# Kernel optimization log

Hardware: AMD Instinct MI355X
Metric: run time of the kernel (lower is better)

Reference implementation:

```python
import jax, jax.numpy as jnp
import numpy as np

N_NODES = 50000
N_EDGES = 800000
D = 128
L = 3


def setup_inputs() -> dict:
    key = jax.random.key(0)
    ks = jax.random.split(key, 8)
    h = jax.random.normal(ks[0], (N_NODES, D), dtype=jnp.float32)
    src = jax.random.randint(ks[1], (N_EDGES,), 0, N_NODES, dtype=jnp.int32)
    dst = jax.random.randint(ks[2], (N_EDGES,), 0, N_NODES, dtype=jnp.int32)
    # MLP weights per GIN layer, scaled ~Glorot to keep activations bounded across layers
    w_scale = 0.05
    W1 = jax.random.normal(ks[3], (L, D, D), dtype=jnp.float32) * w_scale
    b1 = jnp.zeros((L, D), dtype=jnp.float32)
    W2 = jax.random.normal(ks[4], (L, D, D), dtype=jnp.float32) * w_scale
    b2 = jnp.zeros((L, D), dtype=jnp.float32)
    eps = jnp.zeros((L,), dtype=jnp.float32)  # init_eps=0, learnable
    return {"h": h, "src": src, "dst": dst, "W1": W1, "b1": b1, "W2": W2, "b2": b2, "eps": eps}


def reference(h, src, dst, W1, b1, W2, b2, eps):
    # GIN: h <- MLP((1 + eps) * h + sum_{(u->v) in E} h_u) per layer (sum aggregation)
    n = h.shape[0]
    for l in range(W1.shape[0]):
        agg = jax.ops.segment_sum(h[src], dst, num_segments=n)  # [N, D]
        z = (1.0 + eps[l]) * h + agg
        hid = jnp.maximum(z @ W1[l] + b1[l], 0.0)  # Linear + ReLU
        h = hid @ W2[l] + b2[l]                    # Linear
    return h
```

## Files before the change

kernel.cpp:

```cpp
#include <hip/hip_runtime.h>
#include <hip/hip_bf16.h>
#include <stdint.h>

#define N_NODES 50000
#define N_EDGES 800000
#define D 128
#define NLAYER 3
#define NGROUP (N_NODES / 16)
#define CAPG 384
#define GSTRIDE 384
#define MAXCH 12

#define NBKT2 196
#define BCAP 4608
#define EPB_A 2048
#define PA_BLOCKS ((N_EDGES + EPB_A - 1) / EPB_A)

typedef __attribute__((ext_vector_type(8))) short bf16x8;
typedef __attribute__((ext_vector_type(4))) float f32x4;

__device__ __forceinline__ short f2bf(float f) {
    union { float f; uint32_t u; } v; v.f = f;
    uint32_t u = v.u;
    uint32_t r = u + 0x7fffu + ((u >> 16) & 1u);
    return (short)(r >> 16);
}
__device__ __forceinline__ float bf2f(short s) {
    union { uint32_t u; float f; } v;
    v.u = ((uint32_t)(uint16_t)s) << 16;
    return v.f;
}

__global__ void wconv(const float* __restrict__ W1, const float* __restrict__ W2,
                      short* __restrict__ Wswz) {
    int t = blockIdx.x * blockDim.x + threadIdx.x;
    if (t >= NLAYER * 2 * 4 * 8 * 64) return;
    int lane = t & 63;
    int nt   = (t >> 6) & 7;
    int ks   = (t >> 9) & 3;
    int mat  = (t >> 11) & 1;
    int l    = t >> 12;
    const float* W = (mat == 0 ? W1 : W2) + (size_t)l * D * D;
    int n = nt * 16 + (lane & 15);
    short* outp = Wswz + (size_t)t * 8;
#pragma unroll
    for (int j = 0; j < 8; ++j) {
        int k = ks * 32 + (lane >> 4) * 8 + j;
        outp[j] = f2bf(W[k * D + n]);
    }
}

__global__ void h2bf(const float* __restrict__ h, short* __restrict__ hbf) {
    int t = blockIdx.x * blockDim.x + threadIdx.x;
    if (t >= N_NODES * D / 8) return;
    f32x4 a = ((const f32x4*)h)[2 * t];
    f32x4 b = ((const f32x4*)h)[2 * t + 1];
    bf16x8 o;
    o[0] = f2bf(a.x); o[1] = f2bf(a.y); o[2] = f2bf(a.z); o[3] = f2bf(a.w);
    o[4] = f2bf(b.x); o[5] = f2bf(b.y); o[6] = f2bf(b.z); o[7] = f2bf(b.w);
    ((bf16x8*)hbf)[t] = o;
}

__global__ void zero_bcur(int* __restrict__ bcur) {
    if (threadIdx.x < NBKT2) bcur[threadIdx.x] = 0;
}

__global__ __launch_bounds__(256) void packA(const int* __restrict__ src,
                                             const int* __restrict__ dst,
                                             int* __restrict__ bcur,
                                             int* __restrict__ epack) {
    __shared__ int hcnt[NBKT2];
    __shared__ int hbase[NBKT2];
    if (threadIdx.x < NBKT2) hcnt[threadIdx.x] = 0;
    __syncthreads();
    int base = blockIdx.x * EPB_A;
    int end = base + EPB_A; if (end > N_EDGES) end = N_EDGES;
    for (int e = base + threadIdx.x; e < end; e += 256)
        atomicAdd(&hcnt[dst[e] >> 8], 1);
    __syncthreads();
    if (threadIdx.x < NBKT2) {
        int c = hcnt[threadIdx.x];
        hbase[threadIdx.x] = c ? atomicAdd(&bcur[threadIdx.x], c) : 0;
        hcnt[threadIdx.x] = 0;
    }
    __syncthreads();
    for (int e = base + threadIdx.x; e < end; e += 256) {
        int s = src[e], d = dst[e];
        int b = d >> 8;
        int r = atomicAdd(&hcnt[b], 1);
        int slot = hbase[b] + r;
        if (slot < BCAP)
            epack[(size_t)b * BCAP + slot] = (s << 8) | (d & 255);
    }
}

__global__ __launch_bounds__(256) void segB(const int* __restrict__ epack,
                                            const int* __restrict__ bcur,
                                            int* __restrict__ esd,
                                            int* __restrict__ gcnt) {
    __shared__ int image[16 * GSTRIDE];
    __shared__ int cur[16];
    const int b = blockIdx.x;
    int n = bcur[b]; if (n > BCAP) n = BCAP;
    const int* ep = epack + (size_t)b * BCAP;
    const int nG = (NGROUP - b * 16 < 16) ? (NGROUP - b * 16) : 16;

    for (int i = threadIdx.x; i < 16 * GSTRIDE; i += 256) image[i] = 0x80;
    if (threadIdx.x < 16) cur[threadIdx.x] = 0;
    __syncthreads();
    for (int i = threadIdx.x; i < n; i += 256) {
        int e = ep[i];
        int g = (e >> 4) & 15;
        int r = atomicAdd(&cur[g], 1);
        if (r < CAPG) image[g * GSTRIDE + r] = e & ~0xF0;
    }
    __syncthreads();
    if (threadIdx.x < nG) {
        int c = cur[threadIdx.x];
        gcnt[b * 16 + threadIdx.x] = (c > CAPG) ? CAPG : c;
    }
    for (int i = threadIdx.x; i < nG * GSTRIDE; i += 256)
        esd[(size_t)(b * 16) * GSTRIDE + i] = image[i];
}

__global__ __launch_bounds__(256) void gin_layer(const short* __restrict__ hbf,
                                                 const int* __restrict__ gcnt,
                                                 const int* __restrict__ esd,
                                                 const short* __restrict__ Wl,
                                                 const float* __restrict__ b1,
                                                 const float* __restrict__ b2,
                                                 const float* __restrict__ eps, int l,
                                                 float* __restrict__ outf,
                                                 short* __restrict__ outbf, int last) {
    __shared__ union {
        short stg[3][4096];
        struct { short zl[2048]; short hl[2048]; } t;
    } sm;
    __shared__ __align__(8) unsigned char dmask[512];

    const int lane = threadIdx.x & 63;
    const int wid  = threadIdx.x >> 6;
    const int g    = blockIdx.x;
    const int n0   = g * 16;
    const int m    = lane & 15;
    const int kh   = lane >> 4;

    const char* hby = (const char*)hbf;
    const int lo  = g * GSTRIDE;
    int cnt = gcnt[g]; if (cnt > CAPG) cnt = CAPG;
    const int nch = (cnt + 31) >> 5;
    const uint32_t one = 0x3F80u;

    const int sl = lane >> 2;
    const int wq = wid * 64 + (lane & 3) * 16;

    const uint32_t stg_base =
        (uint32_t)(uintptr_t)(__attribute__((address_space(3))) short*)&sm.stg[0][0];

    f32x4 acc[2];
    acc[0] = (f32x4)(0.0f); acc[1] = (f32x4)(0.0f);

#define STAGE(b, rA, rB) do { \
        __builtin_amdgcn_global_load_lds( \
            (const __attribute__((address_space(1))) void*)(hby + (uint32_t)((rA) & ~0xFF) + wq), \
            (__attribute__((address_space(3))) void*)(&sm.stg[(b)][0] + wid * 1024), 16, 0, 0); \
        __builtin_amdgcn_global_load_lds( \
            (const __attribute__((address_space(1))) void*)(hby + (uint32_t)((rB) & ~0xFF) + wq), \
            (__attribute__((address_space(3))) void*)(&sm.stg[(b)][0] + wid * 1024 + 512), 16, 0, 0); \
    } while (0)

    const int* ep = esd + lo;

    int esvA[MAXCH], esvB[MAXCH];
#pragma unroll
    for (int c = 0; c < MAXCH; ++c) {
        esvA[c] = ep[c * 32 + sl];
        esvB[c] = ep[c * 32 + 16 + sl];
    }

    STAGE(0, esvA[0], esvB[0]);
    STAGE(1, esvA[1], esvB[1]);

    if (wid == 0 && (lane & 3) == 0) {
        const int sA = sl, sB = 16 + sl;
        const int pA = ((sA >> 1) & 3) * 8 + 2 * (sA >> 3) + (sA & 1);
        const int pB = ((sB >> 1) & 3) * 8 + 2 * (sB >> 3) + (sB & 1);
#pragma unroll
        for (int c = 0; c < MAXCH; ++c) {
            dmask[c * 32 + pA] = (unsigned char)(esvA[c] & 0xFF);
            dmask[c * 32 + pB] = (unsigned char)(esvB[c] & 0xFF);
        }
    }
    asm volatile("s_waitcnt lgkmcnt(0)" ::: "memory");
    __builtin_amdgcn_s_barrier();

#pragma unroll
    for (int c = 0; c < MAXCH; ++c) {
        if (c >= nch) break;
        if (c + 2 < nch) {
            STAGE((c + 2) % 3, esvA[c + 2], esvB[c + 2]);
            asm volatile("s_waitcnt vmcnt(4)" ::: "memory");
        } else if (c + 1 < nch) {
            asm volatile("s_waitcnt vmcnt(2)" ::: "memory");
        } else {
            asm volatile("s_waitcnt vmcnt(0)" ::: "memory");
        }
        __builtin_amdgcn_sched_barrier(0);

        uint32_t breg = stg_base + (uint32_t)((c % 3) * 8192 + wid * 2048) + lane * 8;
        uint64_t t0, t1, t2, t3;
        asm volatile("ds_read_b64_tr_b16 %0, %1"             : "=v"(t0) : "v"(breg));
        asm volatile("ds_read_b64_tr_b16 %0, %1 offset:512"  : "=v"(t1) : "v"(breg));
        asm volatile("ds_read_b64_tr_b16 %0, %1 offset:1024" : "=v"(t2) : "v"(breg));
        asm volatile("ds_read_b64_tr_b16 %0, %1 offset:1536" : "=v"(t3) : "v"(breg));
        uint2 dm = *(const uint2*)&dmask[c * 32 + kh * 8];
        asm volatile("s_waitcnt lgkmcnt(0)" ::: "memory");
        __builtin_amdgcn_sched_barrier(0);

        union U64 { uint64_t u; uint32_t d[2]; };
        U64 p0, p1, p2, p3; p0.u = t0; p1.u = t1; p2.u = t2; p3.u = t3;
        union { uint32_t w[4]; bf16x8 v; } bf0, bf1;
        bf0.w[0] = (p0.d[0] & 0xFFFFu) | (p0.d[1] << 16);
        bf1.w[0] = (p0.d[0] >> 16) | (p0.d[1] & 0xFFFF0000u);
        bf0.w[1] = (p1.d[0] & 0xFFFFu) | (p1.d[1] << 16);
        bf1.w[1] = (p1.d[0] >> 16) | (p1.d[1] & 0xFFFF0000u);
        bf0.w[2] = (p2.d[0] & 0xFFFFu) | (p2.d[1] << 16);
        bf1.w[2] = (p2.d[0] >> 16) | (p2.d[1] & 0xFFFF0000u);
        bf0.w[3] = (p3.d[0] & 0xFFFFu) | (p3.d[1] << 16);
        bf1.w[3] = (p3.d[0] >> 16) | (p3.d[1] & 0xFFFF0000u);

        bf16x8 am;
#pragma unroll
        for (int e = 0; e < 4; ++e) {
            am[e]     = (((dm.x >> (e * 8)) & 255u) == (uint32_t)m) ? (short)one : (short)0;
            am[e + 4] = (((dm.y >> (e * 8)) & 255u) == (uint32_t)m) ? (short)one : (short)0;
        }
        acc[0] = __builtin_amdgcn_mfma_f32_16x16x32_bf16(am, bf0.v, acc[0], 0, 0, 0);
        acc[1] = __builtin_amdgcn_mfma_f32_16x16x32_bf16(am, bf1.v, acc[1], 0, 0, 0);
    }

    {
        const float se = 1.0f + eps[l];
#pragma unroll
        for (int t = 0; t < 2; ++t) {
            int col = (wid * 2 + t) * 16 + m;
#pragma unroll
            for (int r = 0; r < 4; ++r) {
                int row = n0 + kh * 4 + r;
                acc[t][r] += se * bf2f(hbf[(size_t)row * D + col]);
            }
        }
    }

    __syncthreads();

#pragma unroll
    for (int t = 0; t < 2; ++t) {
        int col = (wid * 2 + t) * 16 + m;
        int gi = col >> 3, ci = col & 7;
#pragma unroll
        for (int r = 0; r < 4; ++r) {
            int row = kh * 4 + r;
            sm.t.zl[row * 128 + ((gi ^ (row & 7)) << 3) + ci] = f2bf(acc[t][r]);
        }
    }
    __syncthreads();

    f32x4 acc1[2];
    acc1[0] = (f32x4)(0.0f); acc1[1] = (f32x4)(0.0f);
#pragma unroll
    for (int ks = 0; ks < 4; ++ks) {
        int gidx = ks * 4 + kh;
        bf16x8 af = *(const bf16x8*)&sm.t.zl[m * 128 + ((gidx ^ (m & 7)) * 8)];
#pragma unroll
        for (int t = 0; t < 2; ++t) {
            int nt = wid * 2 + t;
            bf16x8 bf = *(const bf16x8*)(Wl + ((size_t)(ks * 8 + nt) * 64 + lane) * 8);
            acc1[t] = __builtin_amdgcn_mfma_f32_16x16x32_bf16(af, bf, acc1[t], 0, 0, 0);
        }
    }
#pragma unroll
    for (int t = 0; t < 2; ++t) {
        int col = (wid * 2 + t) * 16 + m;
        float bias = b1[col];
#pragma unroll
        for (int r = 0; r < 4; ++r) {
            int hrow = kh * 4 + r;
            float v = fmaxf(acc1[t][r] + bias, 0.0f);
            sm.t.hl[hrow * 128 + (col ^ ((hrow & 7) << 3))] = f2bf(v);
        }
    }
    __syncthreads();

    f32x4 acc2[2];
    acc2[0] = (f32x4)(0.0f); acc2[1] = (f32x4)(0.0f);
    const short* W2p = Wl + 4 * 8 * 64 * 8;
#pragma unroll
    for (int ks = 0; ks < 4; ++ks) {
        int c0 = ks * 32 + kh * 8;
        bf16x8 af = *(const bf16x8*)&sm.t.hl[m * 128 + (c0 ^ ((m & 7) << 3))];
#pragma unroll
        for (int t = 0; t < 2; ++t) {
            int nt = wid * 2 + t;
            bf16x8 bf = *(const bf16x8*)(W2p + ((size_t)(ks * 8 + nt) * 64 + lane) * 8);
            acc2[t] = __builtin_amdgcn_mfma_f32_16x16x32_bf16(af, bf, acc2[t], 0, 0, 0);
        }
    }
#pragma unroll
    for (int t = 0; t < 2; ++t) {
        int col = (wid * 2 + t) * 16 + m;
        float bias = b2[col];
#pragma unroll
        for (int r = 0; r < 4; ++r) {
            int orow = n0 + kh * 4 + r;
            float v = acc2[t][r] + bias;
            if (last) outf[(size_t)orow * D + col] = v;
            else      outbf[(size_t)orow * D + col] = f2bf(v);
        }
    }
#undef STAGE
}

extern "C" void kernel_launch(void* const* d_in, const int* in_sizes, int n_in,
                              void* d_out, int out_size, void* d_ws, size_t ws_size,
                              hipStream_t stream) {
    const float* h   = (const float*)d_in[0];
    const int*   src = (const int*)d_in[1];
    const int*   dst = (const int*)d_in[2];
    const float* W1  = (const float*)d_in[3];
    const float* b1  = (const float*)d_in[4];
    const float* W2  = (const float*)d_in[5];
    const float* b2  = (const float*)d_in[6];
    const float* eps = (const float*)d_in[7];
    float* out = (float*)d_out;

    char* ws = (char*)d_ws;
    const size_t MB = 1024 * 1024;
    short* hbfA = (short*)ws;
    short* hbfB = (short*)(ws + 13 * MB);
    short* Wswz = (short*)(ws + 26 * MB);
    int*   gcnt = (int*)(ws + 27 * MB);
    int*   bcur = (int*)(ws + 27 * MB + 512 * 1024);
    int*   esd  = (int*)(ws + 28 * MB);
    int*   epack= (int*)(ws + 33 * MB);

    wconv<<<48, 256, 0, stream>>>(W1, W2, Wswz);
    h2bf<<<(N_NODES * D / 8 + 255) / 256, 256, 0, stream>>>(h, hbfA);
    zero_bcur<<<1, 256, 0, stream>>>(bcur);
    packA<<<PA_BLOCKS, 256, 0, stream>>>(src, dst, bcur, epack);
    segB<<<NBKT2, 256, 0, stream>>>(epack, bcur, esd, gcnt);

    const short* hin[3]   = {hbfA, hbfB, hbfA};
    short*      houtbf[3] = {hbfB, hbfA, nullptr};

    for (int l = 0; l < NLAYER; ++l) {
        gin_layer<<<NGROUP, 256, 0, stream>>>(hin[l], gcnt, esd,
                                              Wswz + (size_t)l * 2 * 16384,
                                              b1 + (size_t)l * D, b2 + (size_t)l * D,
                                              eps, l, out, houtbf[l],
                                              l == NLAYER - 1 ? 1 : 0);
    }
}
```

Before: 141.3 us.

## Gather neighbor features as FP8 and convert to bf16 in registers

Writes an extra FP8 copy of node features in the conversion kernel and after each layer, and switches the edge gather from bf16 direct-to-LDS loads to FP8 register loads. Loaded values are converted to bf16 and written to a now double-buffered LDS stage. This halves the bytes moved by the random gather, which is the dominant cost. In exchange it adds an extra output write per layer, conversion ALU work, and a different pipelining scheme, and it lowers the precision of the aggregated neighbor sum, which may hurt accuracy.

```diff
diff --git a/kernel.cpp b/kernel.cpp
--- a/kernel.cpp
+++ b/kernel.cpp
@@ -18,6 +18,7 @@
 
 typedef __attribute__((ext_vector_type(8))) short bf16x8;
 typedef __attribute__((ext_vector_type(4))) float f32x4;
+typedef __attribute__((ext_vector_type(2))) float f32x2;
 
 __device__ __forceinline__ short f2bf(float f) {
     union { float f; uint32_t u; } v; v.f = f;
@@ -29,6 +30,25 @@
     union { uint32_t u; float f; } v;
     v.u = ((uint32_t)(uint16_t)s) << 16;
     return v.f;
+}
+
+__device__ __forceinline__ bf16x8 f8_to_bf16x8(uint2 r) {
+    f32x2 f01 = __builtin_amdgcn_cvt_pk_f32_fp8(r.x, false);
+    f32x2 f23 = __builtin_amdgcn_cvt_pk_f32_fp8(r.x, true);
+    f32x2 f45 = __builtin_amdgcn_cvt_pk_f32_fp8(r.y, false);
+    f32x2 f67 = __builtin_amdgcn_cvt_pk_f32_fp8(r.y, true);
+    uint32_t w0, w1, w2, w3;
+    asm("v_cvt_pk_bf16_f32 %0, %1, %2" : "=v"(w0) : "v"(f01.x), "v"(f01.y));
+    asm("v_cvt_pk_bf16_f32 %0, %1, %2" : "=v"(w1) : "v"(f23.x), "v"(f23.y));
+    asm("v_cvt_pk_bf16_f32 %0, %1, %2" : "=v"(w2) : "v"(f45.x), "v"(f45.y));
+    asm("v_cvt_pk_bf16_f32 %0, %1, %2" : "=v"(w3) : "v"(f67.x), "v"(f67.y));
+    union { uint32_t w[4]; bf16x8 v; } u;
+    u.w[0] = w0; u.w[1] = w1; u.w[2] = w2; u.w[3] = w3;
+    return u.v;
+}
+
+__device__ __forceinline__ unsigned char f2fp8(float f) {
+    return (unsigned char)(__builtin_amdgcn_cvt_pk_fp8_f32(f, f, 0u, false) & 0xFF);
 }
 
 __global__ void wconv(const float* __restrict__ W1, const float* __restrict__ W2,
@@ -50,7 +70,8 @@
     }
 }
 
-__global__ void h2bf(const float* __restrict__ h, short* __restrict__ hbf) {
+__global__ void h2bf(const float* __restrict__ h, short* __restrict__ hbf,
+                     unsigned char* __restrict__ hf8) {
     int t = blockIdx.x * blockDim.x + threadIdx.x;
     if (t >= N_NODES * D / 8) return;
     f32x4 a = ((const f32x4*)h)[2 * t];
@@ -59,6 +80,12 @@
     o[0] = f2bf(a.x); o[1] = f2bf(a.y); o[2] = f2bf(a.z); o[3] = f2bf(a.w);
     o[4] = f2bf(b.x); o[5] = f2bf(b.y); o[6] = f2bf(b.z); o[7] = f2bf(b.w);
     ((bf16x8*)hbf)[t] = o;
+    uint32_t lo = 0, hi = 0;
+    lo = __builtin_amdgcn_cvt_pk_fp8_f32(a.x, a.y, lo, false);
+    lo = __builtin_amdgcn_cvt_pk_fp8_f32(a.z, a.w, lo, true);
+    hi = __builtin_amdgcn_cvt_pk_fp8_f32(b.x, b.y, hi, false);
+    hi = __builtin_amdgcn_cvt_pk_fp8_f32(b.z, b.w, hi, true);
+    ((uint2*)hf8)[t] = make_uint2(lo, hi);
 }
 
 __global__ void zero_bcur(int* __restrict__ bcur) {
@@ -124,6 +151,7 @@
 }
 
 __global__ __launch_bounds__(256) void gin_layer(const short* __restrict__ hbf,
+                                                 const unsigned char* __restrict__ hf8,
                                                  const int* __restrict__ gcnt,
                                                  const int* __restrict__ esd,
                                                  const short* __restrict__ Wl,
@@ -131,9 +159,11 @@
                                                  const float* __restrict__ b2,
                                                  const float* __restrict__ eps, int l,
                                                  float* __restrict__ outf,
-                                                 short* __restrict__ outbf, int last) {
+                                                 short* __restrict__ outbf,
+                                                 unsigned char* __restrict__ outf8,
+                                                 int last) {
     __shared__ union {
-        short stg[3][4096];
+        short stg[2][4096];
         struct { short zl[2048]; short hl[2048]; } t;
     } sm;
     __shared__ __align__(8) unsigned char dmask[512];
@@ -145,29 +175,19 @@
     const int m    = lane & 15;
     const int kh   = lane >> 4;
 
-    const char* hby = (const char*)hbf;
     const int lo  = g * GSTRIDE;
     int cnt = gcnt[g]; if (cnt > CAPG) cnt = CAPG;
     const int nch = (cnt + 31) >> 5;
     const uint32_t one = 0x3F80u;
 
-    const int sl = lane >> 2;
-    const int wq = wid * 64 + (lane & 3) * 16;
+    const int sl  = lane >> 2;
+    const int wq8 = wid * 32 + (lane & 3) * 8;
 
     const uint32_t stg_base =
         (uint32_t)(uintptr_t)(__attribute__((address_space(3))) short*)&sm.stg[0][0];
 
     f32x4 acc[2];
     acc[0] = (f32x4)(0.0f); acc[1] = (f32x4)(0.0f);
-
-#define STAGE(b, rA, rB) do { \
-        __builtin_amdgcn_global_load_lds( \
-            (const __attribute__((address_space(1))) void*)(hby + (uint32_t)((rA) & ~0xFF) + wq), \
-            (__attribute__((address_space(3))) void*)(&sm.stg[(b)][0] + wid * 1024), 16, 0, 0); \
-        __builtin_amdgcn_global_load_lds( \
-            (const __attribute__((address_space(1))) void*)(hby + (uint32_t)((rB) & ~0xFF) + wq), \
-            (__attribute__((address_space(3))) void*)(&sm.stg[(b)][0] + wid * 1024 + 512), 16, 0, 0); \
-    } while (0)
 
     const int* ep = esd + lo;
 
@@ -178,8 +198,20 @@
         esvB[c] = ep[c * 32 + 16 + sl];
     }
 
-    STAGE(0, esvA[0], esvB[0]);
-    STAGE(1, esvA[1], esvB[1]);
+#define LDPAIR(rA, rB, c) do { \
+        rA = *(const uint2*)(hf8 + (((uint32_t)(esvA[(c)] & ~0xFF)) >> 1) + wq8); \
+        rB = *(const uint2*)(hf8 + (((uint32_t)(esvB[(c)] & ~0xFF)) >> 1) + wq8); \
+    } while (0)
+
+    auto cw = [&](int b, uint2 rA, uint2 rB) {
+        short* base = &sm.stg[b][0] + wid * 1024 + lane * 8;
+        *(bf16x8*)base         = f8_to_bf16x8(rA);
+        *(bf16x8*)(base + 512) = f8_to_bf16x8(rB);
+    };
+
+    uint2 rA0, rB0, rA1, rB1;
+    LDPAIR(rA0, rB0, 0);
+    LDPAIR(rA1, rB1, 1);
 
     if (wid == 0 && (lane & 3) == 0) {
         const int sA = sl, sB = 16 + sl;
@@ -194,20 +226,21 @@
     asm volatile("s_waitcnt lgkmcnt(0)" ::: "memory");
     __builtin_amdgcn_s_barrier();
 
+    cw(0, rA0, rB0);
+
 #pragma unroll
     for (int c = 0; c < MAXCH; ++c) {
         if (c >= nch) break;
-        if (c + 2 < nch) {
-            STAGE((c + 2) % 3, esvA[c + 2], esvB[c + 2]);
-            asm volatile("s_waitcnt vmcnt(4)" ::: "memory");
-        } else if (c + 1 < nch) {
-            asm volatile("s_waitcnt vmcnt(2)" ::: "memory");
-        } else {
-            asm volatile("s_waitcnt vmcnt(0)" ::: "memory");
-        }
-        __builtin_amdgcn_sched_barrier(0);
-
-        uint32_t breg = stg_base + (uint32_t)((c % 3) * 8192 + wid * 2048) + lane * 8;
+        if (c + 2 < MAXCH) {
+            if (c & 1) LDPAIR(rA1, rB1, c + 2);
+            else       LDPAIR(rA0, rB0, c + 2);
+        }
+        if (c + 1 < nch) {
+            if ((c + 1) & 1) cw(1, rA1, rB1);
+            else             cw(0, rA0, rB0);
+        }
+
+        uint32_t breg = stg_base + (uint32_t)((c & 1) * 8192 + wid * 2048) + lane * 8;
         uint64_t t0, t1, t2, t3;
         asm volatile("ds_read_b64_tr_b16 %0, %1"             : "=v"(t0) : "v"(breg));
         asm volatile("ds_read_b64_tr_b16 %0, %1 offset:512"  : "=v"(t1) : "v"(breg));
@@ -314,11 +347,15 @@
         for (int r = 0; r < 4; ++r) {
             int orow = n0 + kh * 4 + r;
             float v = acc2[t][r] + bias;
-            if (last) outf[(size_t)orow * D + col] = v;
-            else      outbf[(size_t)orow * D + col] = f2bf(v);
-        }
-    }
-#undef STAGE
+            if (last) {
+                outf[(size_t)orow * D + col] = v;
+            } else {
+                outbf[(size_t)orow * D + col] = f2bf(v);
+                outf8[(size_t)orow * D + col] = f2fp8(v);
+            }
+        }
+    }
+#undef LDPAIR
 }
 
 extern "C" void kernel_launch(void* const* d_in, const int* in_sizes, int n_in,
@@ -338,26 +375,30 @@
     const size_t MB = 1024 * 1024;
     short* hbfA = (short*)ws;
     short* hbfB = (short*)(ws + 13 * MB);
-    short* Wswz = (short*)(ws + 26 * MB);
-    int*   gcnt = (int*)(ws + 27 * MB);
-    int*   bcur = (int*)(ws + 27 * MB + 512 * 1024);
-    int*   esd  = (int*)(ws + 28 * MB);
-    int*   epack= (int*)(ws + 33 * MB);
+    unsigned char* hf8A = (unsigned char*)(ws + 26 * MB);
+    unsigned char* hf8B = (unsigned char*)(ws + 33 * MB);
+    short* Wswz = (short*)(ws + 40 * MB);
+    int*   gcnt = (int*)(ws + 40 * MB + 512 * 1024);
+    int*   bcur = (int*)(ws + 40 * MB + 768 * 1024);
+    int*   esd  = (int*)(ws + 41 * MB);
+    int*   epack= (int*)(ws + 46 * MB);
 
     wconv<<<48, 256, 0, stream>>>(W1, W2, Wswz);
-    h2bf<<<(N_NODES * D / 8 + 255) / 256, 256, 0, stream>>>(h, hbfA);
+    h2bf<<<(N_NODES * D / 8 + 255) / 256, 256, 0, stream>>>(h, hbfA, hf8A);
     zero_bcur<<<1, 256, 0, stream>>>(bcur);
     packA<<<PA_BLOCKS, 256, 0, stream>>>(src, dst, bcur, epack);
     segB<<<NBKT2, 256, 0, stream>>>(epack, bcur, esd, gcnt);
 
-    const short* hin[3]   = {hbfA, hbfB, hbfA};
-    short*      houtbf[3] = {hbfB, hbfA, nullptr};
+    const short*         hin[3]  = {hbfA, hbfB, hbfA};
+    const unsigned char* f8in[3] = {hf8A, hf8B, hf8A};
+    short*         houtbf[3] = {hbfB, hbfA, nullptr};
+    unsigned char* houtf8[3] = {hf8B, hf8A, nullptr};
 
     for (int l = 0; l < NLAYER; ++l) {
-        gin_layer<<<NGROUP, 256, 0, stream>>>(hin[l], gcnt, esd,
+        gin_layer<<<NGROUP, 256, 0, stream>>>(hin[l], f8in[l], gcnt, esd,
                                               Wswz + (size_t)l * 2 * 16384,
                                               b1 + (size_t)l * D, b2 + (size_t)l * D,
-                                              eps, l, out, houtbf[l],
+                                              eps, l, out, houtbf[l], houtf8[l],
                                               l == NLAYER - 1 ? 1 : 0);
     }
 }
```

Result: no change. 143.3 us (+1.5%).
